# Performance work log

Measured on AMD Instinct MI355X. Metric: run time of the kernel, lower is better.

The kernel has to match this reference:

```python
import jax, jax.numpy as jnp
import numpy as np

M1, M2 = 16, 16          # modes1, modes2
CIN, COUT = 32, 32
B, N, TDIM = 8, 4096, 128


def _kgrids():
    # k_x1: [m1], k_x2: [m2] with m1=2*M1, m2=2*M2-1 (matches torch cat of aranges)
    k1 = np.concatenate([np.arange(M1), np.arange(-M1, 0)]).astype(np.float32)
    k2 = np.concatenate([np.arange(M2), np.arange(-(M2 - 1), 0)]).astype(np.float32)
    return jnp.asarray(k1), jnp.asarray(k2)


def _basis(x, k1, k2, sign):
    # x: [B,N,2] -> complex basis [B,N,m1,m2] = exp(sign*2pi*i*(x0*k1 + x1*k2))
    K = x[..., 0, None, None] * k1[:, None] + x[..., 1, None, None] * k2[None, :]
    return jnp.exp(sign * 2j * jnp.pi * K)


def setup_inputs() -> dict:
    key = jax.random.key(0)
    ks = jax.random.split(key, 7)
    scale_w = 1.0 / (CIN * COUT)
    scale_f = 1.0 / (TDIM + 4 * M1 * M2)
    return {
        "u": jax.random.normal(ks[0], (B, CIN, N), jnp.float32),
        "x_in": jax.random.uniform(ks[1], (B, N, 2), dtype=jnp.float32),
        "x_out": jax.random.uniform(ks[2], (B, N, 2), dtype=jnp.float32),
        "t": jax.random.normal(ks[3], (B, TDIM), jnp.float32),
        "w_freq": scale_f * jax.random.normal(ks[4], (TDIM, 4 * M1 * M2), jnp.float32),
        "b_freq": jnp.zeros((1, 4 * M1 * M2), jnp.float32),
        "w1": scale_w * jax.random.uniform(ks[5], (CIN, COUT, M1, M2, 2), dtype=jnp.float32),
        "w2": scale_w * jax.random.uniform(ks[6], (CIN, COUT, M1, M2, 2), dtype=jnp.float32),
    }


def reference(u, x_in, x_out, t, w_freq, b_freq, w1, w2):
    k1, k2 = _kgrids()
    # Freq2dLinear conditioning: [B,TDIM] -> complex [B,M1,M2,2]
    h = (t @ w_freq + b_freq).reshape(t.shape[0], M1, M2, 2, 2)
    emb = h[..., 0] + 1j * h[..., 1]
    emb1, emb2 = emb[..., 0], emb[..., 1]  # each [B,M1,M2]
    w1c = w1[..., 0] + 1j * w1[..., 1]
    w2c = w2[..., 0] + 1j * w2[..., 1]
    # non-uniform forward transform (fft2d)
    basis_in = _basis(x_in, k1, k2, -1.0)  # [B,N,2*M1,2*M2-1]
    u_ft = jnp.einsum('bcn,bnxy->bcxy', u.astype(jnp.complex64), basis_in)
    # emb-conditioned complex mode-wise matmuls
    f1 = jnp.einsum('bixy,ioxy->boxy', u_ft[:, :, :M1, :M2] * emb1[:, None], w1c)
    f2 = jnp.einsum('bixy,ioxy->boxy', u_ft[:, :, -M1:, :M2] * emb2[:, None], w2c)
    out_ft = jnp.concatenate([f1, f2], axis=-2)  # [B,COUT,2*M1,M2]
    # Hermitian extension then non-uniform inverse transform (ifft2d)
    uf2 = jnp.conj(jnp.flip(out_ft[..., 1:], axis=(-1, -2)))
    out_full = jnp.concatenate([out_ft, uf2], axis=-1)  # [B,COUT,2*M1,2*M2-1]
    basis_out = _basis(x_out, k1, k2, 1.0)
    Y = jnp.einsum('bcxy,bnxy->bcn', out_full, basis_out)
    return jnp.real(Y)
```

## Files before the change

kernel.cpp:

```cpp
#include <hip/hip_runtime.h>
#include <hip/hip_bf16.h>


#define NPTS 4096
#define TDIM 128
#define TWO_PI 6.283185307179586f

typedef __attribute__((ext_vector_type(8))) short bf16x8;
typedef __attribute__((ext_vector_type(4))) float f32x4;
typedef unsigned int u32;
typedef unsigned short u16;

__device__ __forceinline__ u32 pack2(float a, float b) {
  __hip_bfloat162 h = __float22bfloat162_rn(make_float2(a, b));
  u32 r; __builtin_memcpy(&r, &h, 4); return r;
}
__device__ __forceinline__ float bflo(u32 u) { return __uint_as_float(u << 16); }
__device__ __forceinline__ float bfhi(u32 u) { return __uint_as_float(u & 0xFFFF0000u); }

__global__ __launch_bounds__(256) void prep1_kernel(
    const float* __restrict__ x_in, u32* __restrict__ E2in, u32* __restrict__ B_pre) {
  const int bid = blockIdx.x;
  const int b = bid & 7, ntile = bid >> 3;
  const int tid = threadIdx.x;
  const int nl = tid & 63, task = tid >> 6;
  const int n = ntile * 64 + nl;
  float2 xv = *(const float2*)&x_in[(size_t)(b * NPTS + n) * 2];
  if (task < 2) {
    #pragma unroll
    for (int k = 0; k < 8; ++k) {
      int y = task * 8 + k;
      float th = TWO_PI * xv.y * (float)y;
      float s, c; __sincosf(th, &s, &c);
      E2in[((b * 16 + y) << 12) + n] = pack2(c, s);
    }
  } else {
    u32* base = B_pre + (size_t)(b * 64 + ntile) * 4096;
    #pragma unroll
    for (int k = 0; k < 16; ++k) {
      int x = (task - 2) * 16 + k;
      float k1x = (x < 16) ? (float)x : (float)(x - 32);
      float th = TWO_PI * xv.x * k1x;
      float s, c; __sincosf(th, &s, &c);
      base[(2 * x) * 64 + nl]     = pack2(c, s);
      base[(2 * x + 1) * 64 + nl] = pack2(-s, c);
    }
  }
}

__global__ __launch_bounds__(256) void uft_kernel(
    const float* __restrict__ u, const u32* __restrict__ E2in,
    const u32* __restrict__ B_pre, float* __restrict__ P) {
  const int bid = blockIdx.x;
  const int b = bid & 7;
  const int rest = bid >> 3;
  const int s = rest & 7;
  const int yq = rest >> 3;
  const int tid = threadIdx.x;
  const int lane = tid & 63, jt = tid >> 6;
  const int colw = lane & 15, kq = lane >> 4;

  __shared__ __align__(16) u16 As[4 * 32 * 128];
  __shared__ __align__(16) u16 Bs[64 * 128];

  f32x4 acc[4][2];
  #pragma unroll
  for (int yl = 0; yl < 4; ++yl)
    #pragma unroll
    for (int m = 0; m < 2; ++m) acc[yl][m] = (f32x4){0.f, 0.f, 0.f, 0.f};

  for (int ch = 0; ch < 8; ++ch) {
    const int n0 = s * 512 + ch * 64;
    const int nt = s * 8 + ch;

    float4 uv[8]; uint4 ev[8]; uint4 bv[4];
    #pragma unroll
    for (int i = 0; i < 8; ++i) {
      int idx = tid + i * 256;
      int y = idx >> 9, c = (idx >> 4) & 31, q = idx & 15;
      uv[i] = *(const float4*)&u[(size_t)(b * 32 + c) * NPTS + n0 + q * 4];
      ev[i] = *(const uint4*)&E2in[((b * 16 + yq * 4 + y) << 12) + n0 + q * 4];
    }
    #pragma unroll
    for (int i = 0; i < 4; ++i) {
      int idx = tid + i * 256;
      int j = idx >> 4, seg = idx & 15;
      bv[i] = *(const uint4*)&B_pre[(size_t)(b * 64 + nt) * 4096 + j * 64 + seg * 4];
    }
    __syncthreads();

    #pragma unroll
    for (int i = 0; i < 8; ++i) {
      int idx = tid + i * 256;
      int y = idx >> 9, c = (idx >> 4) & 31, q = idx & 15;
      const float uu[4] = {uv[i].x, uv[i].y, uv[i].z, uv[i].w};
      const u32 ee[4] = {ev[i].x, ev[i].y, ev[i].z, ev[i].w};
      uint4 w;
      u32* wp = &w.x;
      #pragma unroll
      for (int p2 = 0; p2 < 4; ++p2)
        wp[p2] = pack2(uu[p2] * bflo(ee[p2]), -(uu[p2] * bfhi(ee[p2])));
      *(uint4*)((char*)As + (y * 32 + c) * 256 + ((q * 16) ^ ((c & 7) << 4))) = w;
    }
    #pragma unroll
    for (int i = 0; i < 4; ++i) {
      int idx = tid + i * 256;
      int j = idx >> 4, seg = idx & 15;
      *(uint4*)((char*)Bs + j * 256 + ((seg * 16) ^ ((j & 7) << 4))) = bv[i];
    }
    __syncthreads();

    const int swz = (colw & 7) << 4;
    #pragma unroll
    for (int ks = 0; ks < 4; ++ks) {
      const int kb = ks * 64 + kq * 16;
      bf16x8 fb = *(bf16x8*)((char*)Bs + (jt * 16 + colw) * 256 + (kb ^ swz));
      #pragma unroll
      for (int yl = 0; yl < 4; ++yl) {
        bf16x8 a0 = *(bf16x8*)((char*)As + (yl * 32 + colw) * 256 + (kb ^ swz));
        bf16x8 a1 = *(bf16x8*)((char*)As + (yl * 32 + 16 + colw) * 256 + (kb ^ swz));
        acc[yl][0] = __builtin_amdgcn_mfma_f32_16x16x32_bf16(a0, fb, acc[yl][0], 0, 0, 0);
        acc[yl][1] = __builtin_amdgcn_mfma_f32_16x16x32_bf16(a1, fb, acc[yl][1], 0, 0, 0);
      }
    }
  }

  #pragma unroll
  for (int yl = 0; yl < 4; ++yl) {
    size_t base = (((size_t)s * 8 + b) * 16 + yq * 4 + yl) * 2048;
    #pragma unroll
    for (int m = 0; m < 2; ++m)
      #pragma unroll
      for (int r = 0; r < 4; ++r)
        P[base + (m * 16 + kq * 4 + r) * 64 + jt * 16 + colw] = acc[yl][m][r];
  }
}

__global__ __launch_bounds__(512) void apply_kernel(
    const float* __restrict__ t, const float* __restrict__ w_freq,
    const float* __restrict__ b_freq, const float* __restrict__ w1,
    const float* __restrict__ w2, const float* __restrict__ P,
    u32* __restrict__ A32) {
  const int x = blockIdx.x, b = blockIdx.y;
  const int tid = threadIdx.x;
  const int m1 = x & 15, sel = x >> 4;

  __shared__ float uf_s[32][16][2];
  __shared__ float emb_s[16][2];
  __shared__ float part[512];

  for (int e = tid; e < 1024; e += 512) {
    int i = e >> 5, r = e & 31, yy = r >> 1, comp = r & 1;
    size_t base = (((size_t)(b * 16 + yy)) * 32 + i) * 64 + 2 * x + comp;
    float sacc = 0.f;
    #pragma unroll
    for (int ss = 0; ss < 8; ++ss) sacc += P[base + (size_t)ss * 262144];
    uf_s[i][yy][comp] = sacc;
  }
  {
    int jjl = tid & 31, kc = tid >> 5;
    int yy = jjl >> 1, pp = jjl & 1;
    int jj = ((m1 * 16 + yy) * 2 + sel) * 2 + pp;
    float sv = 0.f;
    #pragma unroll
    for (int k2 = 0; k2 < 8; ++k2) {
      int k = kc * 8 + k2;
      sv += t[b * TDIM + k] * w_freq[k * 1024 + jj];
    }
    part[tid] = sv;
  }
  __syncthreads();
  if (tid < 32) {
    int yy = tid >> 1, pp = tid & 1;
    int jj = ((m1 * 16 + yy) * 2 + sel) * 2 + pp;
    float acc = b_freq[jj];
    #pragma unroll
    for (int c2 = 0; c2 < 16; ++c2) acc += part[c2 * 32 + tid];
    emb_s[yy][pp] = acc;
  }
  __syncthreads();

  int o = tid >> 4, y = tid & 15;
  const float* wsel = sel ? w2 : w1;
  float fr = 0.f, fi = 0.f;
  #pragma unroll 4
  for (int i = 0; i < 32; ++i) {
    float2 w = *(const float2*)&wsel[(size_t)(((i * 32 + o) * 16 + m1) * 16 + y) * 2];
    float ur = uf_s[i][y][0], ui = uf_s[i][y][1];
    fr += ur * w.x - ui * w.y;
    fi += ur * w.y + ui * w.x;
  }
  float er = emb_s[y][0], ei = emb_s[y][1];
  float orr = fr * er - fi * ei;
  float oii = fr * ei + fi * er;
  A32[((b * 31 + y) * 32 + o) * 32 + x] = pack2(orr, oii);
  if (y > 0)
    A32[((b * 31 + (31 - y)) * 32 + o) * 32 + (31 - x)] = pack2(orr, -oii);
}

__global__ __launch_bounds__(256) void inv_kernel(
    const u32* __restrict__ A32, const float* __restrict__ x_out,
    float* __restrict__ Y) {
  const int bid = blockIdx.x;
  const int b = bid & 7;
  const int rest = bid >> 3;
  const int nt = rest & 63;
  const int h = rest >> 6;
  const int n0 = nt * 64;
  const int tid = threadIdx.x;
  const int lane = tid & 63, wv = tid >> 6;
  const int colw = lane & 15, kq = lane >> 4;

  __shared__ __align__(16) u16 Bgr[64 * 64];
  __shared__ __align__(16) u16 Bgi[64 * 64];
  __shared__ u32 e2s[31 * 64];
  __shared__ __align__(16) u16 Asl[16 * 64];

  {
    const int n = tid & 63, Xg = tid >> 6;
    float x0 = x_out[(size_t)(b * NPTS + n0 + n) * 2];
    #pragma unroll
    for (int i = 0; i < 8; ++i) {
      int X = Xg * 8 + i;
      float k1x = (X < 16) ? (float)X : (float)(X - 32);
      float th = TWO_PI * x0 * k1x;
      float s1, c1; __sincosf(th, &s1, &c1);
      int byt = (4 * X) ^ ((n & 7) << 4);
      *(u32*)((char*)Bgr + n * 128 + byt) = pack2(c1, -s1);
      *(u32*)((char*)Bgi + n * 128 + byt) = pack2(s1, c1);
    }
  }
  {
    const int n = tid & 63;
    float x1 = x_out[(size_t)(b * NPTS + n0 + n) * 2 + 1];
    for (int idx = tid; idx < 1984; idx += 256) {
      int y = idx >> 6;
      float k2y = (y < 16) ? (float)y : (float)(y - 31);
      float th = TWO_PI * x1 * k2y;
      float s2, c2; __sincosf(th, &s2, &c2);
      e2s[idx] = pack2(c2, s2);
    }
  }

  const u32* Abase = A32 + (size_t)b * 31 * 1024 + h * 512;
  const bool stager = tid < 128;
  const int cl = tid >> 3, seg = tid & 7;
  uint4 pA = {0u, 0u, 0u, 0u};
  if (stager) pA = *(const uint4*)(Abase + cl * 32 + seg * 4);
  __syncthreads();

  const int brow = wv * 16 + colw;
  bf16x8 bgr[2], bgi[2];
  #pragma unroll
  for (int ks = 0; ks < 2; ++ks) {
    int kb = ks * 64 + kq * 16;
    bgr[ks] = *(bf16x8*)((char*)Bgr + brow * 128 + (kb ^ ((brow & 7) << 4)));
    bgi[ks] = *(bf16x8*)((char*)Bgi + brow * 128 + (kb ^ ((brow & 7) << 4)));
  }

  f32x4 Yh = {0.f, 0.f, 0.f, 0.f};
  const int swz = (colw & 7) << 4;

  #pragma unroll 1
  for (int y = 0; y < 31; ++y) {
    if (stager)
      *(uint4*)((char*)Asl + cl * 128 + ((seg * 16) ^ ((cl & 7) << 4))) = pA;
    __syncthreads();
    if (y < 30 && stager)
      pA = *(const uint4*)(Abase + (y + 1) * 1024 + cl * 32 + seg * 4);

    bf16x8 af0 = *(bf16x8*)((char*)Asl + colw * 128 + ((kq * 16) ^ swz));
    bf16x8 af1 = *(bf16x8*)((char*)Asl + colw * 128 + ((64 + kq * 16) ^ swz));
    f32x4 z = {0.f, 0.f, 0.f, 0.f};
    f32x4 gr = __builtin_amdgcn_mfma_f32_16x16x32_bf16(af0, bgr[0], z, 0, 0, 0);
    gr = __builtin_amdgcn_mfma_f32_16x16x32_bf16(af1, bgr[1], gr, 0, 0, 0);
    f32x4 gi = __builtin_amdgcn_mfma_f32_16x16x32_bf16(af0, bgi[0], z, 0, 0, 0);
    gi = __builtin_amdgcn_mfma_f32_16x16x32_bf16(af1, bgi[1], gi, 0, 0, 0);
    u32 e2 = e2s[y * 64 + brow];
    float c2 = bflo(e2), s2 = bfhi(e2);
    #pragma unroll
    for (int r = 0; r < 4; ++r) Yh[r] += gr[r] * c2 - gi[r] * s2;
    __syncthreads();
  }

  int n = n0 + brow;
  #pragma unroll
  for (int r = 0; r < 4; ++r)
    Y[(size_t)(b * 32 + kq * 4 + r + 16 * h) * NPTS + n] = Yh[r];
}

extern "C" void kernel_launch(void* const* d_in, const int* in_sizes, int n_in,
                              void* d_out, int out_size, void* d_ws, size_t ws_size,
                              hipStream_t stream) {
  const float* u      = (const float*)d_in[0];
  const float* x_in   = (const float*)d_in[1];
  const float* x_out  = (const float*)d_in[2];
  const float* t      = (const float*)d_in[3];
  const float* w_freq = (const float*)d_in[4];
  const float* b_freq = (const float*)d_in[5];
  const float* w1     = (const float*)d_in[6];
  const float* w2     = (const float*)d_in[7];
  float* Y = (float*)d_out;

  u32* E2in  = (u32*)d_ws;
  u32* B_pre = E2in + 524288;
  float* P   = (float*)(B_pre + 2097152);
  u32* A32   = E2in;

  prep1_kernel<<<512, 256, 0, stream>>>(x_in, E2in, B_pre);
  uft_kernel<<<256, 256, 0, stream>>>(u, E2in, B_pre, P);
  apply_kernel<<<dim3(32, 8), 512, 0, stream>>>(t, w_freq, b_freq, w1, w2, P, A32);
  inv_kernel<<<1024, 256, 0, stream>>>(A32, x_out, Y);
}
```

Baseline: 82.46 us.

## Split uft per y-row, prefetch next chunk, batch inverse staging four rows

The uft kernel now gives each block a single y row instead of four. That cuts shared memory and accumulator registers and quadruples the grid to 1024 blocks for better occupancy. Global loads for the next n-chunk are issued before the MFMA loop so they overlap compute. The inverse kernel stages four y rows per sync into a double-buffered LDS tile, which cuts barrier count roughly fourfold. The cost is that u and B_pre are reloaded once per y row rather than once per four rows, raising global traffic.

Result: no change. 83.34 us (+1.1%).

```diff
diff --git a/kernel.cpp b/kernel.cpp
--- a/kernel.cpp
+++ b/kernel.cpp
@@ -55,59 +55,56 @@
   const int b = bid & 7;
   const int rest = bid >> 3;
   const int s = rest & 7;
-  const int yq = rest >> 3;
+  const int y = rest >> 3;
   const int tid = threadIdx.x;
   const int lane = tid & 63, jt = tid >> 6;
   const int colw = lane & 15, kq = lane >> 4;
 
-  __shared__ __align__(16) u16 As[4 * 32 * 128];
+  __shared__ __align__(16) u16 As[32 * 128];
   __shared__ __align__(16) u16 Bs[64 * 128];
 
-  f32x4 acc[4][2];
-  #pragma unroll
-  for (int yl = 0; yl < 4; ++yl)
-    #pragma unroll
-    for (int m = 0; m < 2; ++m) acc[yl][m] = (f32x4){0.f, 0.f, 0.f, 0.f};
-
-  for (int ch = 0; ch < 8; ++ch) {
+  const int cseg = tid & 15;
+  const int crow = tid >> 4;
+
+  f32x4 acc0 = {0.f, 0.f, 0.f, 0.f}, acc1 = {0.f, 0.f, 0.f, 0.f};
+
+  float4 pu[2]; uint4 pe; uint4 pb[4];
+  auto load_regs = [&](int ch) {
     const int n0 = s * 512 + ch * 64;
     const int nt = s * 8 + ch;
-
-    float4 uv[8]; uint4 ev[8]; uint4 bv[4];
-    #pragma unroll
-    for (int i = 0; i < 8; ++i) {
-      int idx = tid + i * 256;
-      int y = idx >> 9, c = (idx >> 4) & 31, q = idx & 15;
-      uv[i] = *(const float4*)&u[(size_t)(b * 32 + c) * NPTS + n0 + q * 4];
-      ev[i] = *(const uint4*)&E2in[((b * 16 + yq * 4 + y) << 12) + n0 + q * 4];
+    #pragma unroll
+    for (int i = 0; i < 2; ++i)
+      pu[i] = *(const float4*)&u[(size_t)(b * 32 + crow + i * 16) * NPTS + n0 + cseg * 4];
+    pe = *(const uint4*)&E2in[((b * 16 + y) << 12) + n0 + cseg * 4];
+    #pragma unroll
+    for (int i = 0; i < 4; ++i)
+      pb[i] = *(const uint4*)&B_pre[(size_t)(b * 64 + nt) * 4096 + (crow + i * 16) * 64 + cseg * 4];
+  };
+  load_regs(0);
+
+  for (int ch = 0; ch < 8; ++ch) {
+    __syncthreads();
+
+    {
+      const u32 ee[4] = {pe.x, pe.y, pe.z, pe.w};
+      #pragma unroll
+      for (int i = 0; i < 2; ++i) {
+        const int c = crow + i * 16;
+        const float uu[4] = {pu[i].x, pu[i].y, pu[i].z, pu[i].w};
+        uint4 w;
+        u32* wp = &w.x;
+        #pragma unroll
+        for (int p2 = 0; p2 < 4; ++p2)
+          wp[p2] = pack2(uu[p2] * bflo(ee[p2]), -(uu[p2] * bfhi(ee[p2])));
+        *(uint4*)((char*)As + c * 256 + ((cseg * 16) ^ ((c & 7) << 4))) = w;
+      }
     }
     #pragma unroll
     for (int i = 0; i < 4; ++i) {
-      int idx = tid + i * 256;
-      int j = idx >> 4, seg = idx & 15;
-      bv[i] = *(const uint4*)&B_pre[(size_t)(b * 64 + nt) * 4096 + j * 64 + seg * 4];
-    }
-    __syncthreads();
-
-    #pragma unroll
-    for (int i = 0; i < 8; ++i) {
-      int idx = tid + i * 256;
-      int y = idx >> 9, c = (idx >> 4) & 31, q = idx & 15;
-      const float uu[4] = {uv[i].x, uv[i].y, uv[i].z, uv[i].w};
-      const u32 ee[4] = {ev[i].x, ev[i].y, ev[i].z, ev[i].w};
-      uint4 w;
-      u32* wp = &w.x;
-      #pragma unroll
-      for (int p2 = 0; p2 < 4; ++p2)
-        wp[p2] = pack2(uu[p2] * bflo(ee[p2]), -(uu[p2] * bfhi(ee[p2])));
-      *(uint4*)((char*)As + (y * 32 + c) * 256 + ((q * 16) ^ ((c & 7) << 4))) = w;
-    }
-    #pragma unroll
-    for (int i = 0; i < 4; ++i) {
-      int idx = tid + i * 256;
-      int j = idx >> 4, seg = idx & 15;
-      *(uint4*)((char*)Bs + j * 256 + ((seg * 16) ^ ((j & 7) << 4))) = bv[i];
-    }
+      const int j = crow + i * 16;
+      *(uint4*)((char*)Bs + j * 256 + ((cseg * 16) ^ ((j & 7) << 4))) = pb[i];
+    }
+    if (ch < 7) load_regs(ch + 1);
     __syncthreads();
 
     const int swz = (colw & 7) << 4;
@@ -115,24 +112,18 @@
     for (int ks = 0; ks < 4; ++ks) {
       const int kb = ks * 64 + kq * 16;
       bf16x8 fb = *(bf16x8*)((char*)Bs + (jt * 16 + colw) * 256 + (kb ^ swz));
-      #pragma unroll
-      for (int yl = 0; yl < 4; ++yl) {
-        bf16x8 a0 = *(bf16x8*)((char*)As + (yl * 32 + colw) * 256 + (kb ^ swz));
-        bf16x8 a1 = *(bf16x8*)((char*)As + (yl * 32 + 16 + colw) * 256 + (kb ^ swz));
-        acc[yl][0] = __builtin_amdgcn_mfma_f32_16x16x32_bf16(a0, fb, acc[yl][0], 0, 0, 0);
-        acc[yl][1] = __builtin_amdgcn_mfma_f32_16x16x32_bf16(a1, fb, acc[yl][1], 0, 0, 0);
-      }
-    }
-  }
-
+      bf16x8 a0 = *(bf16x8*)((char*)As + colw * 256 + (kb ^ swz));
+      bf16x8 a1 = *(bf16x8*)((char*)As + (16 + colw) * 256 + (kb ^ swz));
+      acc0 = __builtin_amdgcn_mfma_f32_16x16x32_bf16(a0, fb, acc0, 0, 0, 0);
+      acc1 = __builtin_amdgcn_mfma_f32_16x16x32_bf16(a1, fb, acc1, 0, 0, 0);
+    }
+  }
+
+  size_t base = (((size_t)s * 8 + b) * 16 + y) * 2048;
   #pragma unroll
-  for (int yl = 0; yl < 4; ++yl) {
-    size_t base = (((size_t)s * 8 + b) * 16 + yq * 4 + yl) * 2048;
-    #pragma unroll
-    for (int m = 0; m < 2; ++m)
-      #pragma unroll
-      for (int r = 0; r < 4; ++r)
-        P[base + (m * 16 + kq * 4 + r) * 64 + jt * 16 + colw] = acc[yl][m][r];
+  for (int r = 0; r < 4; ++r) {
+    P[base + (kq * 4 + r) * 64 + jt * 16 + colw] = acc0[r];
+    P[base + (16 + kq * 4 + r) * 64 + jt * 16 + colw] = acc1[r];
   }
 }
 
@@ -214,7 +205,7 @@
   __shared__ __align__(16) u16 Bgr[64 * 64];
   __shared__ __align__(16) u16 Bgi[64 * 64];
   __shared__ u32 e2s[31 * 64];
-  __shared__ __align__(16) u16 Asl[16 * 64];
+  __shared__ __align__(16) u16 Asl[2][4 * 16 * 64];
 
   {
     const int n = tid & 63, Xg = tid >> 6;
@@ -243,10 +234,18 @@
   }
 
   const u32* Abase = A32 + (size_t)b * 31 * 1024 + h * 512;
-  const bool stager = tid < 128;
-  const int cl = tid >> 3, seg = tid & 7;
-  uint4 pA = {0u, 0u, 0u, 0u};
-  if (stager) pA = *(const uint4*)(Abase + cl * 32 + seg * 4);
+  const int syl0 = tid >> 7;
+  const int scl = (tid >> 3) & 15, sseg = tid & 7;
+  uint4 pA[2];
+  auto loadA = [&](int y0) {
+    #pragma unroll
+    for (int i = 0; i < 2; ++i) {
+      int yy = y0 + syl0 + i * 2;
+      pA[i] = (yy < 31) ? *(const uint4*)(Abase + yy * 1024 + scl * 32 + sseg * 4)
+                        : make_uint4(0u, 0u, 0u, 0u);
+    }
+  };
+  loadA(0);
   __syncthreads();
 
   const int brow = wv * 16 + colw;
@@ -262,25 +261,31 @@
   const int swz = (colw & 7) << 4;
 
   #pragma unroll 1
-  for (int y = 0; y < 31; ++y) {
-    if (stager)
-      *(uint4*)((char*)Asl + cl * 128 + ((seg * 16) ^ ((cl & 7) << 4))) = pA;
+  for (int p = 0; p < 8; ++p) {
+    const int y0 = p * 4;
+    char* buf = (char*)Asl[p & 1];
+    #pragma unroll
+    for (int i = 0; i < 2; ++i) {
+      int yl = syl0 + i * 2;
+      *(uint4*)(buf + (yl * 16 + scl) * 128 + ((sseg * 16) ^ ((scl & 7) << 4))) = pA[i];
+    }
     __syncthreads();
-    if (y < 30 && stager)
-      pA = *(const uint4*)(Abase + (y + 1) * 1024 + cl * 32 + seg * 4);
-
-    bf16x8 af0 = *(bf16x8*)((char*)Asl + colw * 128 + ((kq * 16) ^ swz));
-    bf16x8 af1 = *(bf16x8*)((char*)Asl + colw * 128 + ((64 + kq * 16) ^ swz));
-    f32x4 z = {0.f, 0.f, 0.f, 0.f};
-    f32x4 gr = __builtin_amdgcn_mfma_f32_16x16x32_bf16(af0, bgr[0], z, 0, 0, 0);
-    gr = __builtin_amdgcn_mfma_f32_16x16x32_bf16(af1, bgr[1], gr, 0, 0, 0);
-    f32x4 gi = __builtin_amdgcn_mfma_f32_16x16x32_bf16(af0, bgi[0], z, 0, 0, 0);
-    gi = __builtin_amdgcn_mfma_f32_16x16x32_bf16(af1, bgi[1], gi, 0, 0, 0);
-    u32 e2 = e2s[y * 64 + brow];
-    float c2 = bflo(e2), s2 = bfhi(e2);
-    #pragma unroll
-    for (int r = 0; r < 4; ++r) Yh[r] += gr[r] * c2 - gi[r] * s2;
-    __syncthreads();
+    if (p < 7) loadA(y0 + 4);
+
+    const int ny = (p < 7) ? 4 : 3;
+    for (int yl = 0; yl < ny; ++yl) {
+      bf16x8 af0 = *(bf16x8*)(buf + (yl * 16 + colw) * 128 + ((kq * 16) ^ swz));
+      bf16x8 af1 = *(bf16x8*)(buf + (yl * 16 + colw) * 128 + ((64 + kq * 16) ^ swz));
+      f32x4 z = {0.f, 0.f, 0.f, 0.f};
+      f32x4 gr = __builtin_amdgcn_mfma_f32_16x16x32_bf16(af0, bgr[0], z, 0, 0, 0);
+      gr = __builtin_amdgcn_mfma_f32_16x16x32_bf16(af1, bgr[1], gr, 0, 0, 0);
+      f32x4 gi = __builtin_amdgcn_mfma_f32_16x16x32_bf16(af0, bgi[0], z, 0, 0, 0);
+      gi = __builtin_amdgcn_mfma_f32_16x16x32_bf16(af1, bgi[1], gi, 0, 0, 0);
+      u32 e2 = e2s[(y0 + yl) * 64 + brow];
+      float c2 = bflo(e2), s2 = bfhi(e2);
+      #pragma unroll
+      for (int r = 0; r < 4; ++r) Yh[r] += gr[r] * c2 - gi[r] * s2;
+    }
   }
 
   int n = n0 + brow;
@@ -308,7 +313,7 @@
   u32* A32   = E2in;
 
   prep1_kernel<<<512, 256, 0, stream>>>(x_in, E2in, B_pre);
-  uft_kernel<<<256, 256, 0, stream>>>(u, E2in, B_pre, P);
+  uft_kernel<<<1024, 256, 0, stream>>>(u, E2in, B_pre, P);
   apply_kernel<<<dim3(32, 8), 512, 0, stream>>>(t, w_freq, b_freq, w1, w2, P, A32);
   inv_kernel<<<1024, 256, 0, stream>>>(A32, x_out, Y);
 }
```
